# Optimization experiments

Measured on AMD Instinct MI355X. Metric: run time of the kernel, lower is better.

Reference implementation:

```python
import jax, jax.numpy as jnp
import numpy as np
import math

B, S, F, D, H, L, E, K = 8, 1024, 8, 512, 8, 3, 4, 2
HD = D // H


def _ln(x, g, b, eps=1e-5):
    m = x.mean(-1, keepdims=True)
    v = x.var(-1, keepdims=True)
    return (x - m) / jnp.sqrt(v + eps) * g + b


def _pos_encoding(seq, d):
    pos = jnp.arange(seq, dtype=jnp.float32)[:, None]
    div = jnp.exp(jnp.arange(0, d, 2, dtype=jnp.float32) * (-math.log(10000.0) / d))
    pe = jnp.zeros((seq, d), jnp.float32)
    pe = pe.at[:, 0::2].set(jnp.sin(pos * div))
    pe = pe.at[:, 1::2].set(jnp.cos(pos * div))
    return pe


def setup_inputs() -> dict:
    key = jax.random.key(0)
    ks = iter(jax.random.split(key, 40))

    def w(shape, s=0.02):
        return jax.random.normal(next(ks), shape, jnp.float32) * s

    return {
        "x": jax.random.normal(next(ks), (B, S, F), jnp.float32),
        "Wp": w((D, F)), "bp": jnp.zeros((D,), jnp.float32),
        "femb": w((5, D)),
        "qkv_w": w((L, 3 * D, D)), "qkv_b": jnp.zeros((L, 3 * D), jnp.float32),
        "ow": w((L, D, D)), "ob": jnp.zeros((L, D), jnp.float32),
        "g1": jnp.ones((L, D), jnp.float32), "beta1": jnp.zeros((L, D), jnp.float32),
        "gw": w((L, E, D)), "gb": jnp.zeros((L, E), jnp.float32),
        "ew1": w((L, E, 2 * D, D)), "eb1": jnp.zeros((L, E, 2 * D), jnp.float32),
        "ew2": w((L, E, D, 2 * D)), "eb2": jnp.zeros((L, E, D), jnp.float32),
        "g2": jnp.ones((L, D), jnp.float32), "beta2": jnp.zeros((L, D), jnp.float32),
        "hw": w((3, D)), "hb": jnp.zeros((3,), jnp.float32),
        "freq_idx": 2,
    }


def reference(x, Wp, bp, femb, qkv_w, qkv_b, ow, ob, g1, beta1, gw, gb,
              ew1, eb1, ew2, eb2, g2, beta2, hw, hb, freq_idx):
    # instance norm over time axis (torch std is unbiased -> ddof=1)
    mean = x.mean(axis=1, keepdims=True)
    std = x.std(axis=1, ddof=1, keepdims=True) + 1e-5
    xn = (x - mean) / std

    h = xn @ Wp.T + bp                      # [B,S,D]
    h = h + femb[freq_idx]                  # broadcast freq embedding
    h = h + _pos_encoding(S, D)

    for l in range(L):
        # --- multi-head self-attention ---
        qkv = h @ qkv_w[l].T + qkv_b[l]     # [B,S,3D]
        q, k, v = jnp.split(qkv, 3, axis=-1)
        q = q.reshape(B, S, H, HD).transpose(0, 2, 1, 3)
        k = k.reshape(B, S, H, HD).transpose(0, 2, 1, 3)
        v = v.reshape(B, S, H, HD).transpose(0, 2, 1, 3)
        att = jax.nn.softmax(jnp.einsum('bhqd,bhkd->bhqk', q, k) / math.sqrt(HD), axis=-1)
        o = jnp.einsum('bhqk,bhkd->bhqd', att, v).transpose(0, 2, 1, 3).reshape(B, S, D)
        o = o @ ow[l].T + ob[l]
        h = _ln(h + o, g1[l], beta1[l])

        # --- SparseMoE: top-k softmax gating, renormalized combine ---
        flat = h.reshape(-1, D)                               # [T,D], T=B*S
        probs = jax.nn.softmax(flat @ gw[l].T + gb[l], axis=-1)
        tw, ti = jax.lax.top_k(probs, K)                      # [T,K]
        tw = tw / tw.sum(axis=-1, keepdims=True)
        hid = jax.nn.relu(jnp.einsum('td,efd->tef', flat, ew1[l]) + eb1[l])  # [T,E,2D]
        eo = jnp.einsum('tef,edf->ted', hid, ew2[l]) + eb2[l]                # [T,E,D]
        cw = (jax.nn.one_hot(ti, E, dtype=flat.dtype) * tw[..., None]).sum(1)  # [T,E]
        moe = jnp.einsum('te,ted->td', cw, eo).reshape(B, S, D)
        h = _ln(h + moe, g2[l], beta2[l])

    return h[:, -1, :] @ hw.T + hb           # [B,3] quantiles
```

## Files before the change

kernel.cpp:

```cpp
#include <hip/hip_runtime.h>
#include <hip/hip_bf16.h>
#include <math.h>

typedef __hip_bfloat16 bf16;
typedef __attribute__((ext_vector_type(8))) short short8;
typedef __attribute__((ext_vector_type(4))) short s4v;
typedef __attribute__((ext_vector_type(4))) float f32x4;

constexpr int B_ = 8, S_ = 1024, F_ = 8, D_ = 512, H_ = 8, E_ = 4;
constexpr int T_  = B_ * S_;
constexpr int D3_ = 3 * D_;
constexpr int CAP_ = T_ * 2 + E_ * 128;

__device__ __forceinline__ float b2f(bf16 v) { return __bfloat162float(v); }
__device__ __forceinline__ float ldin(const void* p, size_t i, int bf) {
  return bf ? __bfloat162float(((const bf16*)p)[i]) : ((const float*)p)[i];
}
__device__ __forceinline__ void gload16(const void* g, void* l) {
  __builtin_amdgcn_global_load_lds((const __attribute__((address_space(1))) unsigned int*)g,
                                   (__attribute__((address_space(3))) unsigned int*)l, 16, 0, 0);
}

__global__ void detect_kernel(const void* __restrict__ x, int* __restrict__ flag) {
  if (threadIdx.x == 0 && blockIdx.x == 0) {
    const unsigned short* u = (const unsigned short*)x;
    int c = 0;
    for (int i = 0; i < 256; i += 2) {
      int ex = (u[i] >> 7) & 0xFF;
      if (ex >= 96 && ex <= 144) c++;
    }
    flag[0] = (c >= 64) ? 1 : 0;
  }
}

__global__ __launch_bounds__(256) void convw_kernel(const void* __restrict__ Asrc, size_t offA,
                                                    size_t nA,
                                                    const void* __restrict__ Bsrc, size_t offB,
                                                    bf16* __restrict__ dst,
                                                    const int* __restrict__ flag) {
  const int bf = flag[0];
  size_t i = ((size_t)blockIdx.x * 256 + threadIdx.x) * 8;
  const void* s = Asrc;
  size_t so = offA + i;
  if (i >= nA) { s = Bsrc; so = offB + (i - nA); }
  if (bf) {
    *(short8*)(dst + i) = *(const short8*)((const bf16*)s + so);
  } else {
    const float* sp = (const float*)s + so;
    short8 v;
#pragma unroll
    for (int u = 0; u < 8; u++) { bf16 t = __float2bfloat16(sp[u]); v[u] = *(short*)&t; }
    *(short8*)(dst + i) = v;
  }
}

__global__ __launch_bounds__(256) void instnorm_kernel(const void* __restrict__ x,
                                                       float* __restrict__ xn,
                                                       const int* __restrict__ flag) {
  const int bf = flag[0];
  int b = blockIdx.x / F_, f = blockIdx.x % F_;
  int tid = threadIdx.x;
  __shared__ float red[256];
  const int base = b * S_ * F_ + f;
  float s = 0.f;
  for (int j = tid; j < S_; j += 256) s += ldin(x, base + j * F_, bf);
  red[tid] = s; __syncthreads();
  for (int w = 128; w; w >>= 1) { if (tid < w) red[tid] += red[tid + w]; __syncthreads(); }
  float mean = red[0] / S_;
  __syncthreads();
  float v = 0.f;
  for (int j = tid; j < S_; j += 256) { float d = ldin(x, base + j * F_, bf) - mean; v += d * d; }
  red[tid] = v; __syncthreads();
  for (int w = 128; w; w >>= 1) { if (tid < w) red[tid] += red[tid + w]; __syncthreads(); }
  float inv = 1.f / (sqrtf(red[0] / (float)(S_ - 1)) + 1e-5f);
  for (int j = tid; j < S_; j += 256) xn[base + j * F_] = (ldin(x, base + j * F_, bf) - mean) * inv;
}

__global__ __launch_bounds__(256) void pe_kernel(const void* __restrict__ bp,
                                                 const void* __restrict__ femb,
                                                 const int* __restrict__ freq_idx,
                                                 float* __restrict__ addtab,
                                                 const int* __restrict__ flag) {
  const int bf = flag[0];
  int idx = blockIdx.x * 256 + threadIdx.x;
  int dp = idx & (D_ / 2 - 1);
  int s  = idx / (D_ / 2);
  int d0 = dp * 2;
  int fi = freq_idx[0];
  const float cexp = -9.2103403719761836f / (float)D_;
  float ang = (float)s * expf((float)d0 * cexp);
  float sv, cv;
  sincosf(ang, &sv, &cv);
  addtab[(size_t)s * D_ + d0]     = sv + ldin(bp, d0, bf)     + ldin(femb, (size_t)fi * D_ + d0, bf);
  addtab[(size_t)s * D_ + d0 + 1] = cv + ldin(bp, d0 + 1, bf) + ldin(femb, (size_t)fi * D_ + d0 + 1, bf);
}

constexpr int IPG_ = 8;
__global__ __launch_bounds__(256) void input_proj_kernel(const float* __restrict__ xn,
                                                         const void* __restrict__ Wp,
                                                         const float* __restrict__ addtab,
                                                         float* __restrict__ h,
                                                         bf16* __restrict__ hb16,
                                                         const int* __restrict__ flag) {
  const int bf = flag[0];
  const int tid = threadIdx.x;
  const int d0 = tid * 2;
  const int tbase = blockIdx.x * IPG_;
  float wp0[8], wp1[8];
  if (bf) {
    short8 w0 = *(const short8*)((const bf16*)Wp + (size_t)d0 * F_);
    short8 w1 = *(const short8*)((const bf16*)Wp + (size_t)(d0 + 1) * F_);
#pragma unroll
    for (int f = 0; f < 8; f++) {
      unsigned short u0 = (unsigned short)w0[f], u1 = (unsigned short)w1[f];
      wp0[f] = __bfloat162float(*(bf16*)&u0);
      wp1[f] = __bfloat162float(*(bf16*)&u1);
    }
  } else {
    const float* wpf = (const float*)Wp + (size_t)d0 * F_;
    f32x4 a = *(const f32x4*)(wpf);
    f32x4 b = *(const f32x4*)(wpf + 4);
    f32x4 c = *(const f32x4*)(wpf + 8);
    f32x4 d = *(const f32x4*)(wpf + 12);
#pragma unroll
    for (int f = 0; f < 4; f++) { wp0[f] = a[f]; wp0[4 + f] = b[f]; wp1[f] = c[f]; wp1[4 + f] = d[f]; }
  }
#pragma unroll
  for (int g = 0; g < IPG_; g++) {
    int t = tbase + g;
    int s = t & (S_ - 1);
    const float* xr = xn + (size_t)t * F_;
    f32x4 x0 = *(const f32x4*)xr;
    f32x4 x1 = *(const f32x4*)(xr + 4);
    const float2 at = *(const float2*)(addtab + (size_t)s * D_ + d0);
    float a0 = at.x, a1 = at.y;
#pragma unroll
    for (int f = 0; f < 4; f++) { a0 += x0[f] * wp0[f]; a1 += x0[f] * wp1[f]; }
#pragma unroll
    for (int f = 0; f < 4; f++) { a0 += x1[f] * wp0[4 + f]; a1 += x1[f] * wp1[4 + f]; }
    *(float2*)(h + (size_t)t * D_ + d0) = make_float2(a0, a1);
    bf16 b0 = __float2bfloat16(a0), b1 = __float2bfloat16(a1);
    unsigned pk = (unsigned)(*(unsigned short*)&b0) | ((unsigned)(*(unsigned short*)&b1) << 16);
    *(unsigned*)(hb16 + (size_t)t * D_ + d0) = pk;
  }
}

template <int MODE>
__global__ __launch_bounds__(256) void mfma_gemm(
    const bf16* __restrict__ A, const bf16* __restrict__ Wt,
    const void* __restrict__ bias, size_t boff, void* __restrict__ C_,
    int Kd, int lda, int ldb, int ldc, const int* __restrict__ flag) {
  const int wbf = flag[0];
  __shared__ bf16 As[2][128][32];
  __shared__ bf16 Bs[2][128][32];
  const int tid = threadIdx.x;
  const int ln = tid & 63, wv = tid >> 6;
  int id = blockIdx.x + gridDim.x * blockIdx.y;
  int xcd = id & 7, idq = id >> 3;
  const int n0 = (idq % gridDim.x) * 128;
  const int m0 = (xcd + 8 * (idq / gridDim.x)) * 128;
  const int wr = (wv >> 1) * 64, wc = (wv & 1) * 64;
  const int mrow = ln & 15, quad = ln >> 4;
  const int srow = ln >> 2;
  const int skof = (ln & 3) * 8;
  const int kchunk = Kd / gridDim.z;
  const int kbeg = blockIdx.z * kchunk;
  const int kend = kbeg + kchunk;

  auto stage = [&](int pb, int k0) {
#pragma unroll
    for (int j = 0; j < 2; j++) {
      int row = 16 * (4 * j + wv) + srow;
      gload16(A + (size_t)(m0 + row) * lda + k0 + skof,
              (char*)&As[pb][0][0] + (size_t)(4 * j + wv) * 1024);
    }
#pragma unroll
    for (int j = 0; j < 2; j++) {
      int row = 16 * (4 * j + wv) + srow;
      gload16(Wt + (size_t)(n0 + row) * ldb + k0 + skof,
              (char*)&Bs[pb][0][0] + (size_t)(4 * j + wv) * 1024);
    }
  };

  f32x4 acc[4][4];
#pragma unroll
  for (int i = 0; i < 4; i++)
#pragma unroll
    for (int j = 0; j < 4; j++) acc[i][j] = (f32x4){0.f, 0.f, 0.f, 0.f};

  stage(0, kbeg);
  int p = 0;
  for (int k0 = kbeg; k0 < kend; k0 += 32) {
    __syncthreads();
    if (k0 + 32 < kend) stage(p ^ 1, k0 + 32);
    short8 af[4], bfr[4];
#pragma unroll
    for (int t = 0; t < 4; t++) {
      af[t]  = *(const short8*)&As[p][wr + t * 16 + mrow][quad * 8];
      bfr[t] = *(const short8*)&Bs[p][wc + t * 16 + mrow][quad * 8];
    }
#pragma unroll
    for (int i = 0; i < 4; i++)
#pragma unroll
      for (int j = 0; j < 4; j++)
        acc[i][j] = __builtin_amdgcn_mfma_f32_16x16x32_bf16(af[i], bfr[j], acc[i][j], 0, 0, 0);
    p ^= 1;
  }

  bf16* slice = (MODE == 0) ? (bf16*)C_ + (size_t)blockIdx.z * T_ * D_ : (bf16*)C_;
#pragma unroll
  for (int tj = 0; tj < 4; tj++) {
    int n = n0 + wc + tj * 16 + mrow;
    float bv = (MODE == 3) ? ldin(bias, boff + n, wbf) : 0.f;
#pragma unroll
    for (int ti = 0; ti < 4; ti++) {
      int mbase = m0 + wr + ti * 16 + quad * 4;
#pragma unroll
      for (int r = 0; r < 4; r++) {
        int m = mbase + r;
        float v = acc[ti][tj][r];
        slice[(size_t)m * ldc + n] = __float2bfloat16(MODE == 3 ? v + bv : v);
      }
    }
  }
}

__global__ __launch_bounds__(256) void attn_kernel(const bf16* __restrict__ qkv,
                                                   bf16* __restrict__ o) {
  __shared__ bf16 QP[64][72];
  __shared__ bf16 Ks[64][72];
  __shared__ bf16 Vt[64][72];
  const int tid = threadIdx.x;
  const int ln = tid & 63, wv = tid >> 6;
  const int mrow = ln & 15, quad = ln >> 4;
  const int id = blockIdx.x;
  const int xcd = id & 7, j = id >> 3;
  const int qt = j & 15;
  const int pr = xcd + 8 * (j >> 4);
  const int hh = pr & 7, b = pr >> 3;
  const int q0 = qt * 64;
  const int sr = tid >> 2;
  const int sg = tid & 3;
  const int sc = sg * 8;

  {
    const bf16* src = qkv + (size_t)(b * S_ + q0 + sr) * D3_ + hh * 64;
    *(short8*)&QP[sr][sc]      = *(const short8*)(src + sc);
    *(short8*)&QP[sr][sc + 32] = *(const short8*)(src + sc + 32);
  }
  __syncthreads();
  short8 aq[2];
  aq[0] = *(const short8*)&QP[wv * 16 + mrow][quad * 8];
  aq[1] = *(const short8*)&QP[wv * 16 + mrow][quad * 8 + 32];

  float m_st = -1e30f, l_st = 0.f;
  f32x4 oacc[4];
#pragma unroll
  for (int t = 0; t < 4; t++) oacc[t] = (f32x4){0.f, 0.f, 0.f, 0.f};

  for (int kt = 0; kt < 16; kt++) {
    int k0 = kt * 64;
    __syncthreads();
    {
      const bf16* src = qkv + (size_t)(b * S_ + k0 + sr) * D3_ + D_ + hh * 64;
      *(short8*)&Ks[sr][sc]      = *(const short8*)(src + sc);
      *(short8*)&Ks[sr][sc + 32] = *(const short8*)(src + sc + 32);
    }
    {
      const bf16* src = qkv + (size_t)(b * S_ + k0 + sr) * D3_ + 2 * D_ + hh * 64;
      short8 v0 = *(const short8*)(src + sc);
      short8 v1 = *(const short8*)(src + sc + 32);
      int col0 = sr ^ (sg << 4);
      int col1 = sr ^ (((sg + 4) & 3) << 4);
#pragma unroll
      for (int u = 0; u < 8; u++) {
        *(short*)&Vt[sc + u][col0]      = v0[u];
        *(short*)&Vt[sc + 32 + u][col1] = v1[u];
      }
    }
    __syncthreads();
    f32x4 s[4];
#pragma unroll
    for (int t = 0; t < 4; t++) {
      s[t] = (f32x4){0.f, 0.f, 0.f, 0.f};
#pragma unroll
      for (int ks = 0; ks < 2; ks++) {
        short8 bk = *(const short8*)&Ks[t * 16 + mrow][quad * 8 + ks * 32];
        s[t] = __builtin_amdgcn_mfma_f32_16x16x32_bf16(bk, aq[ks], s[t], 0, 0, 0);
      }
    }
    float rm = s[0][0];
#pragma unroll
    for (int t = 0; t < 4; t++)
#pragma unroll
      for (int r = 0; r < 4; r++) rm = fmaxf(rm, s[t][r]);
    rm *= 0.125f;
    rm = fmaxf(rm, __shfl_xor(rm, 16, 64));
    rm = fmaxf(rm, __shfl_xor(rm, 32, 64));
    float mnew = fmaxf(m_st, rm);
    float alpha = __expf(m_st - mnew);
    m_st = mnew;
    float rs = 0.f;
#pragma unroll
    for (int t = 0; t < 4; t++) {
      s4v pk;
#pragma unroll
      for (int r = 0; r < 4; r++) {
        float p = __expf(s[t][r] * 0.125f - mnew);
        rs += p;
        bf16 tb = __float2bfloat16(p);
        pk[r] = *(short*)&tb;
      }
      *(s4v*)&QP[wv * 16 + mrow][t * 16 + quad * 4] = pk;
    }
    rs += __shfl_xor(rs, 16, 64);
    rs += __shfl_xor(rs, 32, 64);
    l_st = l_st * alpha + rs;
    float af4[4];
#pragma unroll
    for (int r = 0; r < 4; r++) af4[r] = __shfl(alpha, quad * 4 + r, 64);
#pragma unroll
    for (int t = 0; t < 4; t++)
#pragma unroll
      for (int r = 0; r < 4; r++) oacc[t][r] *= af4[r];
    short8 ap[2];
    ap[0] = *(const short8*)&QP[wv * 16 + mrow][quad * 8];
    ap[1] = *(const short8*)&QP[wv * 16 + mrow][quad * 8 + 32];
#pragma unroll
    for (int t = 0; t < 4; t++) {
      int d = t * 16 + mrow;
      int swz = ((d >> 3) & 3) << 4;
#pragma unroll
      for (int ks = 0; ks < 2; ks++) {
        short8 bv = *(const short8*)&Vt[d][(quad * 8 + ks * 32) ^ swz];
        oacc[t] = __builtin_amdgcn_mfma_f32_16x16x32_bf16(ap[ks], bv, oacc[t], 0, 0, 0);
      }
    }
  }
  float linv[4];
#pragma unroll
  for (int r = 0; r < 4; r++) linv[r] = 1.f / __shfl(l_st, quad * 4 + r, 64);
#pragma unroll
  for (int r = 0; r < 4; r++) {
    size_t base = (size_t)(b * S_ + q0 + wv * 16 + quad * 4 + r) * D_ + hh * 64;
#pragma unroll
    for (int t = 0; t < 4; t++)
      o[base + t * 16 + mrow] = __float2bfloat16(oacc[t][r] * linv[r]);
  }
}

__global__ __launch_bounds__(256) void reduce_ln_kernel(float* __restrict__ h,
                                                        bf16* __restrict__ hb16,
                                                        const bf16* __restrict__ ps,
                                                        int nsl, int mode,
                                                        const void* __restrict__ bias,
                                                        size_t boff,
                                                        const float* __restrict__ cw,
                                                        const void* __restrict__ eb2p,
                                                        size_t e2off,
                                                        const void* __restrict__ g,
                                                        const void* __restrict__ beta,
                                                        size_t off,
                                                        const int* __restrict__ flag) {
  const int bf = flag[0];
  int t = blockIdx.x, tid = threadIdx.x;
  __shared__ float r1[256], r2[256];
  const size_t base = (size_t)t * D_;
  float o0 = 0.f, o1 = 0.f;
  for (int s = 0; s < nsl; s++) {
    o0 += b2f(ps[(size_t)s * T_ * D_ + base + tid]);
    o1 += b2f(ps[(size_t)s * T_ * D_ + base + tid + 256]);
  }
  if (mode == 0) {
    o0 += ldin(bias, boff + tid, bf);
    o1 += ldin(bias, boff + tid + 256, bf);
  } else {
#pragma unroll
    for (int e = 0; e < 4; e++) {
      float w = cw[t * 4 + e];
      o0 += w * ldin(eb2p, e2off + e * D_ + tid, bf);
      o1 += w * ldin(eb2p, e2off + e * D_ + tid + 256, bf);
    }
  }
  float* hr = h + base;
  float v0 = hr[tid] + o0;
  float v1 = hr[tid + 256] + o1;
  r1[tid] = v0 + v1;
  r2[tid] = v0 * v0 + v1 * v1;
  __syncthreads();
  for (int w = 128; w; w >>= 1) { if (tid < w) { r1[tid] += r1[tid + w]; r2[tid] += r2[tid + w]; } __syncthreads(); }
  float mean = r1[0] * (1.f / D_);
  float var  = r2[0] * (1.f / D_) - mean * mean;
  float rstd = rsqrtf(var + 1e-5f);
  float n0 = (v0 - mean) * rstd * ldin(g, off + tid, bf) + ldin(beta, off + tid, bf);
  float n1 = (v1 - mean) * rstd * ldin(g, off + tid + 256, bf) + ldin(beta, off + tid + 256, bf);
  hr[tid] = n0;
  hr[tid + 256] = n1;
  hb16[base + tid] = __float2bfloat16(n0);
  hb16[base + tid + 256] = __float2bfloat16(n1);
}

__global__ __launch_bounds__(256) void gate_kernel(const float* __restrict__ hbuf,
                                                   const void* __restrict__ gw, size_t gwoff,
                                                   const void* __restrict__ gb, size_t gboff,
                                                   float* __restrict__ cw,
                                                   int* __restrict__ einfo,
                                                   float* __restrict__ w0a,
                                                   float* __restrict__ w1a,
                                                   const int* __restrict__ flag) {
  const int bf = flag[0];
  int lane = threadIdx.x & 63, wv = threadIdx.x >> 6;
  int t = blockIdx.x * 4 + wv;
  const float* xr = hbuf + (size_t)t * D_;
  float a[4] = {0, 0, 0, 0};
  for (int d = lane; d < D_; d += 64) {
    float xv = xr[d];
#pragma unroll
    for (int e = 0; e < 4; e++) a[e] += xv * ldin(gw, gwoff + e * D_ + d, bf);
  }
#pragma unroll
  for (int e = 0; e < 4; e++)
    for (int off = 32; off; off >>= 1) a[e] += __shfl_xor(a[e], off, 64);
  if (lane == 0) {
    float lg[4];
#pragma unroll
    for (int e = 0; e < 4; e++) lg[e] = a[e] + ldin(gb, gboff + e, bf);
    float m = fmaxf(fmaxf(lg[0], lg[1]), fmaxf(lg[2], lg[3]));
    float p[4], s = 0.f;
#pragma unroll
    for (int e = 0; e < 4; e++) { p[e] = __expf(lg[e] - m); s += p[e]; }
#pragma unroll
    for (int e = 0; e < 4; e++) p[e] /= s;
    int i0 = 0;
    for (int e = 1; e < 4; e++) if (p[e] > p[i0]) i0 = e;
    int i1 = -1;
    for (int e = 0; e < 4; e++) if (e != i0 && (i1 < 0 || p[e] > p[i1])) i1 = e;
    float s2 = p[i0] + p[i1];
    float ww0 = p[i0] / s2, ww1 = p[i1] / s2;
    float outw[4] = {0, 0, 0, 0};
    outw[i0] = ww0; outw[i1] = ww1;
#pragma unroll
    for (int e = 0; e < 4; e++) cw[t * 4 + e] = outw[e];
    einfo[t] = i0 | (i1 << 4);
    w0a[t] = ww0; w1a[t] = ww1;
  }
}

__global__ __launch_bounds__(256) void route_scan_kernel(const int* __restrict__ einfo,
                                                         int* __restrict__ off,
                                                         int* __restrict__ endp,
                                                         int* __restrict__ cur,
                                                         int* __restrict__ tmap) {
  __shared__ int red[4][256];
  int tid = threadIdx.x;
  int c[4] = {0, 0, 0, 0};
  for (int t = tid; t < T_; t += 256) {
    int inf = einfo[t];
    c[inf & 15]++;
    c[(inf >> 4) & 15]++;
  }
#pragma unroll
  for (int e = 0; e < 4; e++) red[e][tid] = c[e];
  __syncthreads();
  for (int w = 128; w; w >>= 1) {
    if (tid < w)
#pragma unroll
      for (int e = 0; e < 4; e++) red[e][tid] += red[e][tid + w];
    __syncthreads();
  }
  if (tid == 0) {
    int o = 0, idx = 0;
#pragma unroll
    for (int e = 0; e < 4; e++) {
      int cnt = red[e][0];
      off[e] = o;
      endp[e] = o + cnt;
      cur[e] = 0;
      int nt = (cnt + 127) >> 7;
      for (int i = 0; i < nt; i++) tmap[1 + idx++] = e | (i << 8);
      o += nt << 7;
    }
    tmap[0] = idx;
  }
}

__global__ __launch_bounds__(256) void scatter_kernel(const int* __restrict__ einfo,
                                                      const float* __restrict__ w0a,
                                                      const float* __restrict__ w1a,
                                                      const int* __restrict__ off,
                                                      int* __restrict__ cur,
                                                      int* __restrict__ pack,
                                                      float* __restrict__ wlist) {
  int t = blockIdx.x * 256 + threadIdx.x;
  int lane = threadIdx.x & 63;
  int inf = einfo[t];
#pragma unroll
  for (int rank = 0; rank < 2; rank++) {
    int my_e = (rank == 0) ? (inf & 15) : ((inf >> 4) & 15);
    float w = (rank == 0) ? w0a[t] : w1a[t];
#pragma unroll
    for (int e = 0; e < 4; e++) {
      bool p = (my_e == e);
      unsigned long long mask = __ballot(p);
      if (!mask) continue;
      int leader = __ffsll((long long)mask) - 1;
      int base = 0;
      if (lane == leader) base = atomicAdd(&cur[e], (int)__popcll(mask));
      base = __shfl(base, leader, 64);
      if (p) {
        int pos = off[e] + base + (int)__popcll(mask & ((1ULL << lane) - 1ULL));
        pack[pos] = t * 2 + rank;
        wlist[pos] = w;
      }
    }
  }
}

__global__ __launch_bounds__(256) void moe_mat1_kernel(
    const bf16* __restrict__ A, const bf16* __restrict__ Wt,
    const void* __restrict__ bias, size_t boff, bf16* __restrict__ hid,
    const int* __restrict__ off, const int* __restrict__ endp,
    const int* __restrict__ pack, const float* __restrict__ wlist,
    const int* __restrict__ tmap, const int* __restrict__ flag) {
  const int wbf = flag[0];
  int id = blockIdx.x + 8 * blockIdx.y;
  int xcd = id & 7, idq = id >> 3;
  int wx = idq & 7, wy = xcd + 8 * (idq >> 3);
  if (wy >= tmap[0]) return;
  int ent = tmap[1 + wy];
  const int e = ent & 255, mt = ent >> 8;
  const int o = off[e], en = endp[e];
  const int n0 = wx * 128;
  __shared__ bf16 As[2][128][32];
  __shared__ bf16 Bs[2][128][32];
  const int tid = threadIdx.x;
  const int ln = tid & 63, wv = tid >> 6;
  const int m0 = o + mt * 128;
  const int wr = (wv >> 1) * 64, wc = (wv & 1) * 64;
  const int mrow = ln & 15, quad = ln >> 4;
  const int srow = ln >> 2;
  const int skof = (ln & 3) * 8;
  int tokr[2];
#pragma unroll
  for (int j = 0; j < 2; j++) {
    int pos = m0 + 16 * (4 * j + wv) + srow;
    tokr[j] = pack[min(pos, en - 1)] >> 1;
  }
  const size_t wbase = (size_t)e * 1024 * 512;

  auto stage = [&](int pb, int k0) {
#pragma unroll
    for (int j = 0; j < 2; j++)
      gload16(A + (size_t)tokr[j] * 512 + k0 + skof,
              (char*)&As[pb][0][0] + (size_t)(4 * j + wv) * 1024);
#pragma unroll
    for (int j = 0; j < 2; j++) {
      int row = 16 * (4 * j + wv) + srow;
      gload16(Wt + wbase + (size_t)(n0 + row) * 512 + k0 + skof,
              (char*)&Bs[pb][0][0] + (size_t)(4 * j + wv) * 1024);
    }
  };

  f32x4 acc[4][4];
#pragma unroll
  for (int i = 0; i < 4; i++)
#pragma unroll
    for (int j = 0; j < 4; j++) acc[i][j] = (f32x4){0.f, 0.f, 0.f, 0.f};

  stage(0, 0);
  int p = 0;
  for (int k0 = 0; k0 < 512; k0 += 32) {
    __syncthreads();
    if (k0 + 32 < 512) stage(p ^ 1, k0 + 32);
    short8 af[4], bfr[4];
#pragma unroll
    for (int t = 0; t < 4; t++) {
      af[t]  = *(const short8*)&As[p][wr + t * 16 + mrow][quad * 8];
      bfr[t] = *(const short8*)&Bs[p][wc + t * 16 + mrow][quad * 8];
    }
#pragma unroll
    for (int i = 0; i < 4; i++)
#pragma unroll
      for (int j = 0; j < 4; j++)
        acc[i][j] = __builtin_amdgcn_mfma_f32_16x16x32_bf16(af[i], bfr[j], acc[i][j], 0, 0, 0);
    p ^= 1;
  }

#pragma unroll
  for (int ti = 0; ti < 4; ti++) {
#pragma unroll
    for (int r = 0; r < 4; r++) {
      int pos = m0 + wr + ti * 16 + quad * 4 + r;
      float w = (pos < en) ? wlist[pos] : 0.f;
#pragma unroll
      for (int tj = 0; tj < 4; tj++) {
        int ncol = n0 + wc + tj * 16 + mrow;
        float v = acc[ti][tj][r] + ldin(bias, boff + e * 1024 + ncol, wbf);
        hid[(size_t)pos * 1024 + ncol] = __float2bfloat16(fmaxf(v, 0.f) * w);
      }
    }
  }
}

__global__ __launch_bounds__(256) void moe_mat2_kernel(
    const bf16* __restrict__ hid, const bf16* __restrict__ Wt,
    bf16* __restrict__ psl,
    const int* __restrict__ off, const int* __restrict__ endp,
    const int* __restrict__ pack, const int* __restrict__ tmap,
    const int* __restrict__ flag) {
  int id = blockIdx.x + 4 * blockIdx.y;
  int xcd = id & 7, idq = id >> 3;
  int wx = idq & 3, wy = xcd + 8 * (idq >> 2);
  if (wy >= tmap[0]) return;
  int ent = tmap[1 + wy];
  const int e = ent & 255, mt = ent >> 8;
  const int o = off[e], en = endp[e];
  const int n0 = wx * 128;
  __shared__ bf16 As[2][128][32];
  __shared__ bf16 Bs[2][128][32];
  const int tid = threadIdx.x;
  const int ln = tid & 63, wv = tid >> 6;
  const int m0 = o + mt * 128;
  const int wr = (wv >> 1) * 64, wc = (wv & 1) * 64;
  const int mrow = ln & 15, quad = ln >> 4;
  const int srow = ln >> 2;
  const int skof = (ln & 3) * 8;
  const int kbeg = blockIdx.z * 512;
  const size_t wbase = (size_t)e * 512 * 1024;

  auto stage = [&](int pb, int k0) {
#pragma unroll
    for (int j = 0; j < 2; j++) {
      int row = 16 * (4 * j + wv) + srow;
      gload16(hid + (size_t)(m0 + row) * 1024 + k0 + skof,
              (char*)&As[pb][0][0] + (size_t)(4 * j + wv) * 1024);
    }
#pragma unroll
    for (int j = 0; j < 2; j++) {
      int row = 16 * (4 * j + wv) + srow;
      gload16(Wt + wbase + (size_t)(n0 + row) * 1024 + k0 + skof,
              (char*)&Bs[pb][0][0] + (size_t)(4 * j + wv) * 1024);
    }
  };

  f32x4 acc[4][4];
#pragma unroll
  for (int i = 0; i < 4; i++)
#pragma unroll
    for (int j = 0; j < 4; j++) acc[i][j] = (f32x4){0.f, 0.f, 0.f, 0.f};

  stage(0, kbeg);
  int p = 0;
  for (int k0 = kbeg; k0 < kbeg + 512; k0 += 32) {
    __syncthreads();
    if (k0 + 32 < kbeg + 512) stage(p ^ 1, k0 + 32);
    short8 af[4], bfr[4];
#pragma unroll
    for (int t = 0; t < 4; t++) {
      af[t]  = *(const short8*)&As[p][wr + t * 16 + mrow][quad * 8];
      bfr[t] = *(const short8*)&Bs[p][wc + t * 16 + mrow][quad * 8];
    }
#pragma unroll
    for (int i = 0; i < 4; i++)
#pragma unroll
      for (int j = 0; j < 4; j++)
        acc[i][j] = __builtin_amdgcn_mfma_f32_16x16x32_bf16(af[i], bfr[j], acc[i][j], 0, 0, 0);
    p ^= 1;
  }

#pragma unroll
  for (int ti = 0; ti < 4; ti++) {
#pragma unroll
    for (int r = 0; r < 4; r++) {
      int pos = m0 + wr + ti * 16 + quad * 4 + r;
      if (pos < en) {
        int pk = pack[pos];
        int tok = pk >> 1, rank = pk & 1;
        bf16* dst = psl + (size_t)(rank * 2 + blockIdx.z) * T_ * D_ + (size_t)tok * D_;
#pragma unroll
        for (int tj = 0; tj < 4; tj++) {
          int ncol = n0 + wc + tj * 16 + mrow;
          dst[ncol] = __float2bfloat16(acc[ti][tj][r]);
        }
      }
    }
  }
}

__global__ __launch_bounds__(256) void head_kernel(const float* __restrict__ hbuf,
                                                   const void* __restrict__ hw,
                                                   const void* __restrict__ hb,
                                                   void* __restrict__ out,
                                                   const int* __restrict__ flag) {
  const int bf = flag[0];
  int bq = blockIdx.x, tid = threadIdx.x;
  int b = bq / 3, q = bq % 3;
  __shared__ float red[256];
  const float* xr = hbuf + (size_t)(b * S_ + (S_ - 1)) * D_;
  float sacc = xr[tid] * ldin(hw, (size_t)q * D_ + tid, bf)
             + xr[tid + 256] * ldin(hw, (size_t)q * D_ + tid + 256, bf);
  red[tid] = sacc; __syncthreads();
  for (int w = 128; w; w >>= 1) { if (tid < w) red[tid] += red[tid + w]; __syncthreads(); }
  if (tid == 0) {
    float r = red[0] + ldin(hb, q, bf);
    if (bf) ((bf16*)out)[bq] = __float2bfloat16(r);
    else    ((float*)out)[bq] = r;
  }
}

extern "C" void kernel_launch(void* const* d_in, const int* in_sizes, int n_in,
                              void* d_out, int out_size, void* d_ws, size_t ws_size,
                              hipStream_t stream) {
  const void* x    = d_in[0];
  const void* Wp   = d_in[1];
  const void* bp   = d_in[2];
  const void* femb = d_in[3];
  const void* qkvw = d_in[4];
  const void* qkvb = d_in[5];
  const void* ow   = d_in[6];
  const void* ob   = d_in[7];
  const void* g1   = d_in[8];
  const void* be1  = d_in[9];
  const void* gw   = d_in[10];
  const void* gb   = d_in[11];
  const void* ew1  = d_in[12];
  const void* eb1  = d_in[13];
  const void* ew2  = d_in[14];
  const void* eb2  = d_in[15];
  const void* g2   = d_in[16];
  const void* be2  = d_in[17];
  const void* hw   = d_in[18];
  const void* hb   = d_in[19];
  const int*  freq = (const int*)d_in[20];

  int*   flag  = (int*)d_ws;
  int*   off   = flag + 64;
  int*   endp  = off + 4;
  int*   cur   = endp + 4;
  int*   einfo = flag + 128;
  float* w0a   = (float*)(einfo + T_);
  float* w1a   = w0a + T_;
  int*   pack  = (int*)(w1a + T_);
  float* wlist = (float*)(pack + CAP_);
  int*   tmap  = (int*)(wlist + CAP_);
  float* xn    = (float*)(tmap + 160);
  float* h     = xn + 65536;
  float* cw    = h + (size_t)T_ * D_;
  bf16*  hb16  = (bf16*)(cw + (size_t)T_ * E_);
  bf16*  R     = hb16 + (size_t)T_ * D_;
  bf16*  qkvb16 = R;
  bf16*  ao    = R + (size_t)T_ * D3_;
  bf16*  hid   = R;
  bf16*  psl   = R + (size_t)CAP_ * 1024;
  bf16*  wcvt  = psl + (size_t)4 * T_ * D_;
  bf16*  wq    = wcvt;
  bf16*  wo    = wcvt + (size_t)D3_ * D_;
  bf16*  we1   = wcvt;
  bf16*  we2   = wcvt + (size_t)E_ * 1024 * 512;
  float* addtab = (float*)R;

  constexpr size_t NQ = (size_t)D3_ * D_;
  constexpr size_t NO = (size_t)D_ * D_;
  constexpr size_t NE = (size_t)E_ * 1024 * 512;

  detect_kernel<<<1, 64, 0, stream>>>(x, flag);
  instnorm_kernel<<<B_ * F_, 256, 0, stream>>>(x, xn, flag);
  pe_kernel<<<(S_ * D_ / 2) / 256, 256, 0, stream>>>(bp, femb, freq, addtab, flag);
  input_proj_kernel<<<T_ / IPG_, 256, 0, stream>>>(xn, Wp, addtab, h, hb16, flag);

  for (int l = 0; l < 3; l++) {
    convw_kernel<<<(NQ + NO) / 2048, 256, 0, stream>>>(
        qkvw, (size_t)l * NQ, NQ, ow, (size_t)l * NO, wcvt, flag);
    mfma_gemm<3><<<dim3(D3_ / 128, T_ / 128), 256, 0, stream>>>(
        hb16, wq, qkvb, (size_t)l * D3_, qkvb16, D_, D_, D_, D3_, flag);
    attn_kernel<<<B_ * H_ * (S_ / 64), 256, 0, stream>>>(qkvb16, ao);
    mfma_gemm<0><<<dim3(D_ / 128, T_ / 128, 2), 256, 0, stream>>>(
        ao, wo, nullptr, 0, psl, D_, D_, D_, D_, flag);
    reduce_ln_kernel<<<T_, 256, 0, stream>>>(
        h, hb16, psl, 2, 0, ob, (size_t)l * D_, nullptr, nullptr, 0,
        g1, be1, (size_t)l * D_, flag);
    gate_kernel<<<T_ / 4, 256, 0, stream>>>(h, gw, (size_t)l * E_ * D_, gb, (size_t)l * E_,
                                            cw, einfo, w0a, w1a, flag);
    route_scan_kernel<<<1, 256, 0, stream>>>(einfo, off, endp, cur, tmap);
    scatter_kernel<<<T_ / 256, 256, 0, stream>>>(einfo, w0a, w1a, off, cur, pack, wlist);
    convw_kernel<<<(NE + NE) / 2048, 256, 0, stream>>>(
        ew1, (size_t)l * NE, NE, ew2, (size_t)l * NE, wcvt, flag);
    moe_mat1_kernel<<<dim3(8, 136), 256, 0, stream>>>(
        hb16, we1, eb1, (size_t)l * E_ * 1024, hid,
        off, endp, pack, wlist, tmap, flag);
    moe_mat2_kernel<<<dim3(4, 136, 2), 256, 0, stream>>>(
        hid, we2, psl, off, endp, pack, tmap, flag);
    reduce_ln_kernel<<<T_, 256, 0, stream>>>(
        h, hb16, psl, 4, 1, nullptr, 0, cw, eb2, (size_t)l * E_ * D_,
        g2, be2, (size_t)l * D_, flag);
  }

  head_kernel<<<24, 256, 0, stream>>>(h, hw, hb, d_out, flag);
}
```

Before: 886.5 us.

## Triple-buffer LDS staging in MFMA GEMMs with vmcnt-based waits

Converts the dense GEMM and both MoE expert GEMMs from double to triple-buffered global-to-LDS staging, prefetching two K-steps ahead. The full __syncthreads is replaced with a partial s_waitcnt vmcnt plus a raw barrier, so the loads for the next tile can stay in flight while the current tile is computed. The new stage is issued after the LDS fragment reads, which shortens the exposed memory latency per iteration. It costs 50% more shared memory per block, which may lower occupancy. The hand-written vmcnt count must also match the number of loads issued per stage; if it does not, correctness is at risk.

```diff
diff --git a/kernel.cpp b/kernel.cpp
--- a/kernel.cpp
+++ b/kernel.cpp
@@ -151,8 +151,8 @@
     const void* __restrict__ bias, size_t boff, void* __restrict__ C_,
     int Kd, int lda, int ldb, int ldc, const int* __restrict__ flag) {
   const int wbf = flag[0];
-  __shared__ bf16 As[2][128][32];
-  __shared__ bf16 Bs[2][128][32];
+  __shared__ bf16 As[3][128][32];
+  __shared__ bf16 Bs[3][128][32];
   const int tid = threadIdx.x;
   const int ln = tid & 63, wv = tid >> 6;
   int id = blockIdx.x + gridDim.x * blockIdx.y;
@@ -189,22 +189,29 @@
     for (int j = 0; j < 4; j++) acc[i][j] = (f32x4){0.f, 0.f, 0.f, 0.f};
 
   stage(0, kbeg);
+  stage(1, kbeg + 32);
   int p = 0;
   for (int k0 = kbeg; k0 < kend; k0 += 32) {
-    __syncthreads();
-    if (k0 + 32 < kend) stage(p ^ 1, k0 + 32);
+    if (k0 + 32 < kend) asm volatile("s_waitcnt vmcnt(4)" ::: "memory");
+    else                asm volatile("s_waitcnt vmcnt(0)" ::: "memory");
+    __builtin_amdgcn_s_barrier();
+    __builtin_amdgcn_sched_barrier(0);
     short8 af[4], bfr[4];
 #pragma unroll
     for (int t = 0; t < 4; t++) {
       af[t]  = *(const short8*)&As[p][wr + t * 16 + mrow][quad * 8];
       bfr[t] = *(const short8*)&Bs[p][wc + t * 16 + mrow][quad * 8];
     }
+    if (k0 + 64 < kend) {
+      int ps = (p == 0) ? 2 : p - 1;
+      stage(ps, k0 + 64);
+    }
 #pragma unroll
     for (int i = 0; i < 4; i++)
 #pragma unroll
       for (int j = 0; j < 4; j++)
         acc[i][j] = __builtin_amdgcn_mfma_f32_16x16x32_bf16(af[i], bfr[j], acc[i][j], 0, 0, 0);
-    p ^= 1;
+    p = (p == 2) ? 0 : p + 1;
   }
 
   bf16* slice = (MODE == 0) ? (bf16*)C_ + (size_t)blockIdx.z * T_ * D_ : (bf16*)C_;
@@ -531,8 +538,8 @@
   const int e = ent & 255, mt = ent >> 8;
   const int o = off[e], en = endp[e];
   const int n0 = wx * 128;
-  __shared__ bf16 As[2][128][32];
-  __shared__ bf16 Bs[2][128][32];
+  __shared__ bf16 As[3][128][32];
+  __shared__ bf16 Bs[3][128][32];
   const int tid = threadIdx.x;
   const int ln = tid & 63, wv = tid >> 6;
   const int m0 = o + mt * 128;
@@ -568,22 +575,29 @@
     for (int j = 0; j < 4; j++) acc[i][j] = (f32x4){0.f, 0.f, 0.f, 0.f};
 
   stage(0, 0);
+  stage(1, 32);
   int p = 0;
   for (int k0 = 0; k0 < 512; k0 += 32) {
-    __syncthreads();
-    if (k0 + 32 < 512) stage(p ^ 1, k0 + 32);
+    if (k0 + 32 < 512) asm volatile("s_waitcnt vmcnt(4)" ::: "memory");
+    else               asm volatile("s_waitcnt vmcnt(0)" ::: "memory");
+    __builtin_amdgcn_s_barrier();
+    __builtin_amdgcn_sched_barrier(0);
     short8 af[4], bfr[4];
 #pragma unroll
     for (int t = 0; t < 4; t++) {
       af[t]  = *(const short8*)&As[p][wr + t * 16 + mrow][quad * 8];
       bfr[t] = *(const short8*)&Bs[p][wc + t * 16 + mrow][quad * 8];
     }
+    if (k0 + 64 < 512) {
+      int ps = (p == 0) ? 2 : p - 1;
+      stage(ps, k0 + 64);
+    }
 #pragma unroll
     for (int i = 0; i < 4; i++)
 #pragma unroll
       for (int j = 0; j < 4; j++)
         acc[i][j] = __builtin_amdgcn_mfma_f32_16x16x32_bf16(af[i], bfr[j], acc[i][j], 0, 0, 0);
-    p ^= 1;
+    p = (p == 2) ? 0 : p + 1;
   }
 
 #pragma unroll
@@ -616,8 +630,8 @@
   const int e = ent & 255, mt = ent >> 8;
   const int o = off[e], en = endp[e];
   const int n0 = wx * 128;
-  __shared__ bf16 As[2][128][32];
-  __shared__ bf16 Bs[2][128][32];
+  __shared__ bf16 As[3][128][32];
+  __shared__ bf16 Bs[3][128][32];
   const int tid = threadIdx.x;
   const int ln = tid & 63, wv = tid >> 6;
   const int m0 = o + mt * 128;
@@ -650,22 +664,29 @@
     for (int j = 0; j < 4; j++) acc[i][j] = (f32x4){0.f, 0.f, 0.f, 0.f};
 
   stage(0, kbeg);
+  stage(1, kbeg + 32);
   int p = 0;
   for (int k0 = kbeg; k0 < kbeg + 512; k0 += 32) {
-    __syncthreads();
-    if (k0 + 32 < kbeg + 512) stage(p ^ 1, k0 + 32);
+    if (k0 + 32 < kbeg + 512) asm volatile("s_waitcnt vmcnt(4)" ::: "memory");
+    else                      asm volatile("s_waitcnt vmcnt(0)" ::: "memory");
+    __builtin_amdgcn_s_barrier();
+    __builtin_amdgcn_sched_barrier(0);
     short8 af[4], bfr[4];
 #pragma unroll
     for (int t = 0; t < 4; t++) {
       af[t]  = *(const short8*)&As[p][wr + t * 16 + mrow][quad * 8];
       bfr[t] = *(const short8*)&Bs[p][wc + t * 16 + mrow][quad * 8];
     }
+    if (k0 + 64 < kbeg + 512) {
+      int ps = (p == 0) ? 2 : p - 1;
+      stage(ps, k0 + 64);
+    }
 #pragma unroll
     for (int i = 0; i < 4; i++)
 #pragma unroll
       for (int j = 0; j < 4; j++)
         acc[i][j] = __builtin_amdgcn_mfma_f32_16x16x32_bf16(af[i], bfr[j], acc[i][j], 0, 0, 0);
-    p ^= 1;
+    p = (p == 2) ? 0 : p + 1;
   }
 
 #pragma unroll
```

Result: faster. 850.3 us (-4.1%).
